# Kernel optimization log

Measured on AMD Instinct MI355X. Metric: run time of the kernel, lower is better.

The kernel has to match this reference:

```python
import jax, jax.numpy as jnp
import numpy as np
import math

B, C, D, NH, L, DFF = 128, 112, 512, 8, 13, 1920
DK = D // NH  # 64
_pos = np.arange(64)
_ranks, _files = _pos // 8, _pos % 8
RIDX = np.clip(_ranks[:, None] - _ranks[None, :], -7, 7) + 7  # [64,64] rel-rank bucket
FIDX = np.clip(_files[:, None] - _files[None, :], -7, 7) + 7  # [64,64] rel-file bucket
DIAG = _ranks + _files        # [64] in [0,14]
ADIAG = _ranks - _files + 7   # [64] in [0,14]


def _ln(x, g, b):
    m = jnp.mean(x, -1, keepdims=True)
    v = jnp.mean((x - m) ** 2, -1, keepdims=True)
    return (x - m) * jax.lax.rsqrt(v + 1e-5) * g + b


def setup_inputs() -> dict:
    key = jax.random.key(0)
    ks = iter(jax.random.split(key, 40))
    nrm = lambda *s: jax.random.normal(next(ks), s, jnp.float32) * 0.02
    return dict(
        x=jax.random.normal(next(ks), (B, C, 8, 8), jnp.float32),
        conv_w=nrm(C, D), conv_b=jnp.zeros(D),
        cls_token=nrm(1, 1, D),
        abs_pos=nrm(1, 64, D),
        file_emb=nrm(8, D), rank_emb=nrm(8, D),
        diag_emb=nrm(15, D), anti_diag_emb=nrm(15, D),
        ln1_g=jnp.ones((L, D)), ln1_b=jnp.zeros((L, D)),
        wq=nrm(L, D, D), bq=jnp.zeros((L, D)),
        wk=nrm(L, D, D), bk=jnp.zeros((L, D)),
        wv=nrm(L, D, D), bv=jnp.zeros((L, D)),
        wo=nrm(L, D, D), bo=jnp.zeros((L, D)),
        rel_bias=nrm(L, 15, 15, NH),
        ln2_g=jnp.ones((L, D)), ln2_b=jnp.zeros((L, D)),
        w_ff1=nrm(L, D, 2 * DFF), b_ff1=jnp.zeros((L, 2 * DFF)),
        w_ff2=nrm(L, DFF, D), b_ff2=jnp.zeros((L, D)),
        out_g=jnp.ones(D), out_b=jnp.zeros(D),
        vw1=nrm(D, D // 2), vb1=jnp.zeros(D // 2),
        vw2=nrm(D // 2, 128), vb2=jnp.zeros(128),
        vw3=nrm(128, 3), vb3=jnp.zeros(3),
        pw=nrm(D, 72), pb=jnp.zeros(72),
    )


def reference(x, conv_w, conv_b, cls_token, abs_pos, file_emb, rank_emb, diag_emb, anti_diag_emb,
              ln1_g, ln1_b, wq, bq, wk, bk, wv, bv, wo, bo, rel_bias, ln2_g, ln2_b,
              w_ff1, b_ff1, w_ff2, b_ff2, out_g, out_b,
              vw1, vb1, vw2, vb2, vw3, vb3, pw, pb):
    Bc = x.shape[0]
    # 1x1 conv == channel-wise linear; flatten spatial (row-major: s = rank*8 + file)
    tok = jnp.einsum('bcs,cd->bsd', x.reshape(Bc, C, 64), conv_w) + conv_b  # [B,64,D]
    pos = abs_pos + file_emb[_files] + rank_emb[_ranks] + diag_emb[DIAG] + anti_diag_emb[ADIAG]
    tok = tok + pos
    h = jnp.concatenate([jnp.broadcast_to(cls_token, (Bc, 1, D)), tok], axis=1)  # [B,65,D]
    scale = 1.0 / math.sqrt(DK)

    def block(hx, p):
        g1, b1, Wq, Bq, Wk, Bk, Wv, Bv, Wo, Bo, rb, g2, b2, W1, B1, W2, B2 = p
        n = _ln(hx, g1, b1)
        q = (n @ Wq + Bq).reshape(Bc, 65, NH, DK).transpose(0, 2, 1, 3)
        k = (n @ Wk + Bk).reshape(Bc, 65, NH, DK).transpose(0, 2, 1, 3)
        v = (n @ Wv + Bv).reshape(Bc, 65, NH, DK).transpose(0, 2, 1, 3)
        # gather relative-position bias [64,64,H] -> [H,65,65] with zero row/col for CLS
        bias = jnp.pad(jnp.transpose(rb[RIDX, FIDX], (2, 0, 1)), ((0, 0), (1, 0), (1, 0)))
        scores = jnp.einsum('bhqd,bhkd->bhqk', q, k) * scale + bias[None]
        a = jax.nn.softmax(scores, axis=-1)
        ctx = jnp.einsum('bhqk,bhkd->bhqd', a, v).transpose(0, 2, 1, 3).reshape(Bc, 65, D)
        hx = hx + ctx @ Wo + Bo
        n2 = _ln(hx, g2, b2)
        u = n2 @ W1 + B1
        u1, u2 = jnp.split(u, 2, axis=-1)
        hx = hx + (jax.nn.gelu(u1, approximate=False) * u2) @ W2 + B2
        return hx, None

    params = (ln1_g, ln1_b, wq, bq, wk, bk, wv, bv, wo, bo, rel_bias,
              ln2_g, ln2_b, w_ff1, b_ff1, w_ff2, b_ff2)
    h, _ = jax.lax.scan(block, h, params)
    h = _ln(h, out_g, out_b)
    cls = h[:, 0]
    v1 = jax.nn.gelu(cls @ vw1 + vb1, approximate=False)
    v2 = jax.nn.gelu(v1 @ vw2 + vb2, approximate=False)
    value = v2 @ vw3 + vb3                 # WDL logits [B,3]
    policy = (h[:, 1:] @ pw + pb).reshape(Bc, -1)  # [B, 64*72]
    return policy, value
```

## Files before the change

### kernel.cpp

```cpp
#include <hip/hip_runtime.h>
#include <stdint.h>

#define NLAYER 13
#define DMODEL 512
#define SEQ    65
#define BATCH  128
#define MROWS  (BATCH*SEQ)
#define NHEAD  8
#define DFFH   1920

typedef __bf16 bf16x8 __attribute__((ext_vector_type(8)));
typedef float  f32x4  __attribute__((ext_vector_type(4)));

__device__ __forceinline__ float bf2f(unsigned short u) {
    union { unsigned int i; float f; } c; c.i = ((unsigned int)u) << 16; return c.f;
}
__device__ __forceinline__ unsigned short f2bf(float f) {
    union { float f; unsigned int i; } c; c.f = f;
    unsigned int u = c.i;
    u += 0x7fffu + ((u >> 16) & 1u);
    return (unsigned short)(u >> 16);
}
__device__ __forceinline__ float gelu_exact(float x) {
    return 0.5f * x * (1.0f + erff(x * 0.70710678118654752f));
}

#define GLOAD16(gp, lp) __builtin_amdgcn_global_load_lds( \
    (const __attribute__((address_space(1))) unsigned int*)(gp), \
    (__attribute__((address_space(3))) unsigned int*)(lp), 16, 0, 0)

__global__ __launch_bounds__(256) void transpose_f32_bf16(
    const float* __restrict__ src, unsigned short* __restrict__ dst,
    int R, int C, int Cpad, long srcLS, long dstLS, int rowOff)
{
    __shared__ float tile[32][33];
    int l  = blockIdx.z;
    int c0 = blockIdx.x * 32, r0 = blockIdx.y * 32;
    const float* s = src + (long)l * srcLS;
    unsigned short* d = dst + (long)l * dstLS;
    int tx = threadIdx.x, ty = threadIdx.y;
#pragma unroll
    for (int k = 0; k < 4; k++) {
        int r = r0 + ty + 8*k, c = c0 + tx;
        float v = (r < R && c < C) ? s[(long)r * C + c] : 0.0f;
        tile[ty + 8*k][tx] = v;
    }
    __syncthreads();
#pragma unroll
    for (int k = 0; k < 4; k++) {
        int c = c0 + ty + 8*k, r = r0 + tx;
        if (c < Cpad && r < R)
            d[(long)(rowOff + c) * R + r] = f2bf(tile[tx][ty + 8*k]);
    }
}

__global__ __launch_bounds__(256) void stack_bias_kernel(
    const float* __restrict__ bq, const float* __restrict__ bk,
    const float* __restrict__ bv, float* __restrict__ bqkv)
{
    int idx = blockIdx.x * 256 + threadIdx.x;
    if (idx >= NLAYER * 1536) return;
    int l = idx / 1536, r = idx - l * 1536;
    float v;
    if (r < 512)       v = bq[l*512 + r];
    else if (r < 1024) v = bk[l*512 + r - 512];
    else               v = bv[l*512 + r - 1024];
    bqkv[idx] = v;
}

__global__ __launch_bounds__(256) void embed_kernel(
    const float* __restrict__ x, const float* __restrict__ conv_w,
    const float* __restrict__ conv_b, const float* __restrict__ cls_tok,
    const float* __restrict__ abs_pos, const float* __restrict__ file_emb,
    const float* __restrict__ rank_emb, const float* __restrict__ diag_emb,
    const float* __restrict__ adiag_emb, float* __restrict__ h)
{
    int b = blockIdx.y, sg = blockIdx.x, t = threadIdx.x;
    if (sg == 8) {
        for (int d = t; d < 512; d += 256)
            h[(long)b * SEQ * 512 + d] = cls_tok[d];
        return;
    }
    __shared__ float xs[112][8];
    for (int idx = t; idx < 112*8; idx += 256) {
        int c = idx >> 3, j = idx & 7;
        xs[c][j] = x[((long)b*112 + c)*64 + sg*8 + j];
    }
    __syncthreads();
    int d0 = t, d1 = t + 256;
    float acc0[8] = {}, acc1[8] = {};
    for (int c = 0; c < 112; c++) {
        float w0 = conv_w[c*512 + d0], w1 = conv_w[c*512 + d1];
#pragma unroll
        for (int j = 0; j < 8; j++) { acc0[j] += xs[c][j]*w0; acc1[j] += xs[c][j]*w1; }
    }
#pragma unroll
    for (int j = 0; j < 8; j++) {
        int sq = sg*8 + j, r = sq >> 3, f = sq & 7;
        long row = ((long)b * SEQ + 1 + sq) * 512;
        h[row + d0] = acc0[j] + conv_b[d0] + abs_pos[sq*512+d0] + file_emb[f*512+d0]
                    + rank_emb[r*512+d0] + diag_emb[(r+f)*512+d0] + adiag_emb[(r-f+7)*512+d0];
        h[row + d1] = acc1[j] + conv_b[d1] + abs_pos[sq*512+d1] + file_emb[f*512+d1]
                    + rank_emb[r*512+d1] + diag_emb[(r+f)*512+d1] + adiag_emb[(r-f+7)*512+d1];
    }
}

__global__ __launch_bounds__(256) void ln_kernel(
    const float* __restrict__ hx, const float* __restrict__ g,
    const float* __restrict__ bb, unsigned short* __restrict__ o)
{
    int row  = blockIdx.x * 4 + (threadIdx.x >> 6);
    int lane = threadIdx.x & 63;
    const float4* xr = (const float4*)(hx + (long)row * 512);
    float4 v0 = xr[lane], v1 = xr[lane + 64];
    float s  = v0.x+v0.y+v0.z+v0.w + v1.x+v1.y+v1.z+v1.w;
    float s2 = v0.x*v0.x+v0.y*v0.y+v0.z*v0.z+v0.w*v0.w
             + v1.x*v1.x+v1.y*v1.y+v1.z*v1.z+v1.w*v1.w;
    for (int off = 32; off; off >>= 1) { s += __shfl_xor(s, off); s2 += __shfl_xor(s2, off); }
    float mean = s * (1.0f/512.0f);
    float var  = s2 * (1.0f/512.0f) - mean*mean;
    float rs   = rsqrtf(var + 1e-5f);
    const float4* gr = (const float4*)g; const float4* br = (const float4*)bb;
    float4 g0 = gr[lane], g1 = gr[lane+64], b0 = br[lane], b1 = br[lane+64];
    ushort4 o0, o1;
    o0.x = f2bf((v0.x-mean)*rs*g0.x + b0.x);
    o0.y = f2bf((v0.y-mean)*rs*g0.y + b0.y);
    o0.z = f2bf((v0.z-mean)*rs*g0.z + b0.z);
    o0.w = f2bf((v0.w-mean)*rs*g0.w + b0.w);
    o1.x = f2bf((v1.x-mean)*rs*g1.x + b1.x);
    o1.y = f2bf((v1.y-mean)*rs*g1.y + b1.y);
    o1.z = f2bf((v1.z-mean)*rs*g1.z + b1.z);
    o1.w = f2bf((v1.w-mean)*rs*g1.w + b1.w);
    ushort4* orow = (ushort4*)(o + (long)row * 512);
    orow[lane] = o0; orow[lane + 64] = o1;
}

template<int MODE>
__global__ __launch_bounds__(256) void gemm128(
    const unsigned short* __restrict__ A, const unsigned short* __restrict__ Bt,
    const float* __restrict__ bias, const float* __restrict__ res,
    void* __restrict__ out, int K, int ldo)
{
    __shared__ __attribute__((aligned(16))) unsigned short As[128*32];
    __shared__ __attribute__((aligned(16))) unsigned short Bs[128*32];
    int m0 = blockIdx.y * 128;
    int bn = blockIdx.x;
    int tid = threadIdx.x;
    int lane = tid & 63, w = tid >> 6;
    int quad = lane >> 4, col = lane & 15;

    int srow = tid >> 2;
    int sc8  = (tid & 3) * 8;

    int br0, br1;
    if (MODE == 2) {
        br0 = bn*64 + srow;
        br1 = 1920 + bn*64 + srow;
    } else {
        br0 = bn*128 + srow;
        br1 = bn*128 + srow + 64;
    }
    const unsigned short* Arow0 = A + (long)(m0 + srow) * K + sc8;
    const unsigned short* Arow1 = A + (long)(m0 + srow + 64) * K + sc8;
    const unsigned short* Brow0 = Bt + (long)br0 * K + sc8;
    const unsigned short* Brow1 = Bt + (long)br1 * K + sc8;
    unsigned short* lAs0 = &As[srow*32 + sc8];
    unsigned short* lAs1 = &As[(srow+64)*32 + sc8];
    unsigned short* lBs0 = &Bs[srow*32 + sc8];
    unsigned short* lBs1 = &Bs[(srow+64)*32 + sc8];

    f32x4 acc[2][8] = {};

    for (int k0 = 0; k0 < K; k0 += 32) {
        GLOAD16(Arow0 + k0, lAs0);
        GLOAD16(Arow1 + k0, lAs1);
        GLOAD16(Brow0 + k0, lBs0);
        GLOAD16(Brow1 + k0, lBs1);
        __syncthreads();
        bf16x8 af[2], bfr[8];
#pragma unroll
        for (int i = 0; i < 2; i++)
            af[i] = *(const bf16x8*)(&As[(w*32 + i*16 + col)*32 + quad*8]);
#pragma unroll
        for (int t = 0; t < 8; t++)
            bfr[t] = *(const bf16x8*)(&Bs[(t*16 + col)*32 + quad*8]);
#pragma unroll
        for (int i = 0; i < 2; i++)
#pragma unroll
            for (int t = 0; t < 8; t++)
                acc[i][t] = __builtin_amdgcn_mfma_f32_16x16x32_bf16(af[i], bfr[t], acc[i][t], 0, 0, 0);
        __syncthreads();
    }

    if (MODE == 2) {
        unsigned short* O = (unsigned short*)out;
        int gn0 = bn * 64;
#pragma unroll
        for (int i = 0; i < 2; i++)
#pragma unroll
        for (int t = 0; t < 4; t++) {
            int c = t*16 + col;
            float b1v = bias[gn0 + c];
            float b2v = bias[1920 + gn0 + c];
#pragma unroll
            for (int r = 0; r < 4; r++) {
                int m = m0 + w*32 + i*16 + quad*4 + r;
                float u1 = acc[i][t][r]   + b1v;
                float u2 = acc[i][t+4][r] + b2v;
                O[(long)m * DFFH + gn0 + c] = f2bf(gelu_exact(u1) * u2);
            }
        }
        return;
    }
    int n0 = bn * 128;
#pragma unroll
    for (int i = 0; i < 2; i++)
#pragma unroll
    for (int t = 0; t < 8; t++) {
        int cg = n0 + t*16 + col;
        float bv = (MODE == 3) ? (cg < 72 ? bias[cg] : 0.0f) : bias[cg];
#pragma unroll
        for (int r = 0; r < 4; r++) {
            int m = m0 + w*32 + i*16 + quad*4 + r;
            float v = acc[i][t][r] + bv;
            if (MODE == 0) {
                ((unsigned short*)out)[(long)m * ldo + cg] = f2bf(v);
            } else if (MODE == 1) {
                ((float*)out)[(long)m * ldo + cg] = res[(long)m * ldo + cg] + v;
            } else {
                if (cg < 72) {
                    int b2 = m / 65, s = m - b2 * 65;
                    if (s > 0)
                        ((float*)out)[(long)b2 * 4608 + (s - 1) * 72 + cg] = v;
                }
            }
        }
    }
}

__global__ __launch_bounds__(256) void attn_mfma_kernel(
    const unsigned short* __restrict__ qkv,
    const float* __restrict__ rel_bias,
    unsigned short* __restrict__ ctx,
    int layer)
{
    constexpr int QS = 72;
    constexpr int VS = 104;
    constexpr int SS = 68;
    constexpr int PS = 104;
    __shared__ __attribute__((aligned(16))) unsigned short Qs[80*QS];
    __shared__ __attribute__((aligned(16))) unsigned short Ks[80*QS];
    __shared__ __attribute__((aligned(16))) unsigned short Vt[64*VS];
    __shared__ __attribute__((aligned(16))) float Sf[65*SS];
    __shared__ __attribute__((aligned(16))) unsigned short Pb[80*PS];
    __shared__ float bias_s[225];

    int h = blockIdx.x, b = blockIdx.y, t = threadIdx.x;
    int lane = t & 63, w = t >> 6;
    int quad = lane >> 4, col = lane & 15;

    for (int i = t; i < 225; i += 256)
        bias_s[i] = rel_bias[((long)layer*225 + i)*8 + h];

    for (int i = t; i < 65*8; i += 256) {
        int s = i >> 3, c8 = (i & 7) * 8;
        const unsigned short* row = qkv + ((long)(b*65+s))*1536 + h*64 + c8;
        int4 qv = *(const int4*)(row);
        int4 kv = *(const int4*)(row + 512);
        int4 vv = *(const int4*)(row + 1024);
        unsigned short qsc[8];
        const unsigned short* qp = (const unsigned short*)&qv;
#pragma unroll
        for (int j = 0; j < 8; j++) qsc[j] = f2bf(bf2f(qp[j]) * 0.125f);
        *(int4*)&Qs[s*QS + c8] = *(const int4*)qsc;
        *(int4*)&Ks[s*QS + c8] = kv;
        const unsigned short* vp = (const unsigned short*)&vv;
#pragma unroll
        for (int j = 0; j < 8; j++) Vt[(c8+j)*VS + s] = vp[j];
    }
    for (int i = t; i < 64*31; i += 256) {
        int d = i / 31, s = 65 + i % 31;
        Vt[d*VS + s] = 0;
    }
    __syncthreads();

    for (int tt = w; tt < 25; tt += 4) {
        int mi = tt / 5, nj = tt % 5;
        f32x4 acc = {};
        bf16x8 a0 = *(const bf16x8*)&Qs[(mi*16+col)*QS + quad*8];
        bf16x8 b0 = *(const bf16x8*)&Ks[(nj*16+col)*QS + quad*8];
        acc = __builtin_amdgcn_mfma_f32_16x16x32_bf16(a0, b0, acc, 0, 0, 0);
        bf16x8 a1 = *(const bf16x8*)&Qs[(mi*16+col)*QS + 32 + quad*8];
        bf16x8 b1 = *(const bf16x8*)&Ks[(nj*16+col)*QS + 32 + quad*8];
        acc = __builtin_amdgcn_mfma_f32_16x16x32_bf16(a1, b1, acc, 0, 0, 0);
#pragma unroll
        for (int r = 0; r < 4; r++) {
            int qi = mi*16 + quad*4 + r, kj = nj*16 + col;
            if (qi < 65 && kj < 65) {
                float v = acc[r];
                if (qi >= 1 && kj >= 1) {
                    int i2 = qi - 1, j2 = kj - 1;
                    int dr = (i2 >> 3) - (j2 >> 3) + 7;
                    int df = (i2 & 7) - (j2 & 7) + 7;
                    v += bias_s[dr*15 + df];
                }
                Sf[qi*SS + kj] = v;
            }
        }
    }
    __syncthreads();

    for (int r = w; r < 65; r += 4) {
        float x0 = Sf[r*SS + lane];
        float x1 = (lane == 0) ? Sf[r*SS + 64] : -1e30f;
        float mx = fmaxf(x0, x1);
        for (int off = 32; off; off >>= 1) mx = fmaxf(mx, __shfl_xor(mx, off));
        float e0 = __expf(x0 - mx);
        float e1 = (lane == 0) ? __expf(x1 - mx) : 0.0f;
        float sm = e0 + e1;
        for (int off = 32; off; off >>= 1) sm += __shfl_xor(sm, off);
        float inv = 1.0f / sm;
        Pb[r*PS + lane] = f2bf(e0 * inv);
        if (lane == 0)  Pb[r*PS + 64] = f2bf(e1 * inv);
        if (lane >= 1 && lane <= 31) Pb[r*PS + 64 + lane] = 0;
    }
    __syncthreads();

    for (int tt = w; tt < 20; tt += 4) {
        int mi = tt >> 2, dj = tt & 3;
        f32x4 acc = {};
#pragma unroll
        for (int ks = 0; ks < 3; ks++) {
            bf16x8 a  = *(const bf16x8*)&Pb[(mi*16+col)*PS + ks*32 + quad*8];
            bf16x8 bb = *(const bf16x8*)&Vt[(dj*16+col)*VS + ks*32 + quad*8];
            acc = __builtin_amdgcn_mfma_f32_16x16x32_bf16(a, bb, acc, 0, 0, 0);
        }
#pragma unroll
        for (int r = 0; r < 4; r++) {
            int qi = mi*16 + quad*4 + r;
            if (qi < 65)
                ctx[((long)(b*65+qi))*512 + h*64 + dj*16 + col] = f2bf(acc[r]);
        }
    }
}

__global__ __launch_bounds__(256) void value_head_kernel(
    const unsigned short* __restrict__ hn,
    const float* __restrict__ vw1, const float* __restrict__ vb1,
    const float* __restrict__ vw2, const float* __restrict__ vb2,
    const float* __restrict__ vw3, const float* __restrict__ vb3,
    float* __restrict__ outv)
{
    int b = blockIdx.x, t = threadIdx.x;
    __shared__ float cls[512], v1[256], v2[128];
    for (int d = t; d < 512; d += 256) cls[d] = bf2f(hn[(long)b * SEQ * 512 + d]);
    __syncthreads();
    {
        float a = vb1[t];
        for (int c = 0; c < 512; c++) a += cls[c] * vw1[c*256 + t];
        v1[t] = gelu_exact(a);
    }
    __syncthreads();
    if (t < 128) {
        float a = vb2[t];
        for (int c = 0; c < 256; c++) a += v1[c] * vw2[c*128 + t];
        v2[t] = gelu_exact(a);
    }
    __syncthreads();
    if (t < 3) {
        float a = vb3[t];
        for (int c = 0; c < 128; c++) a += v2[c] * vw3[c*3 + t];
        outv[b*3 + t] = a;
    }
}

extern "C" void kernel_launch(void* const* d_in, const int* in_sizes, int n_in,
                              void* d_out, int out_size, void* d_ws, size_t ws_size,
                              hipStream_t stream)
{
    (void)in_sizes; (void)n_in; (void)out_size; (void)ws_size;
    const float* x        = (const float*)d_in[0];
    const float* conv_w   = (const float*)d_in[1];
    const float* conv_b   = (const float*)d_in[2];
    const float* cls_tok  = (const float*)d_in[3];
    const float* abs_pos  = (const float*)d_in[4];
    const float* file_emb = (const float*)d_in[5];
    const float* rank_emb = (const float*)d_in[6];
    const float* diag_emb = (const float*)d_in[7];
    const float* adiag    = (const float*)d_in[8];
    const float* ln1_g    = (const float*)d_in[9];
    const float* ln1_b    = (const float*)d_in[10];
    const float* wq       = (const float*)d_in[11];
    const float* bq       = (const float*)d_in[12];
    const float* wk       = (const float*)d_in[13];
    const float* bk       = (const float*)d_in[14];
    const float* wv       = (const float*)d_in[15];
    const float* bv       = (const float*)d_in[16];
    const float* wo       = (const float*)d_in[17];
    const float* bo       = (const float*)d_in[18];
    const float* rel_bias = (const float*)d_in[19];
    const float* ln2_g    = (const float*)d_in[20];
    const float* ln2_b    = (const float*)d_in[21];
    const float* w_ff1    = (const float*)d_in[22];
    const float* b_ff1    = (const float*)d_in[23];
    const float* w_ff2    = (const float*)d_in[24];
    const float* b_ff2    = (const float*)d_in[25];
    const float* out_g    = (const float*)d_in[26];
    const float* out_b    = (const float*)d_in[27];
    const float* vw1      = (const float*)d_in[28];
    const float* vb1      = (const float*)d_in[29];
    const float* vw2      = (const float*)d_in[30];
    const float* vb2      = (const float*)d_in[31];
    const float* vw3      = (const float*)d_in[32];
    const float* vb3      = (const float*)d_in[33];
    const float* pw       = (const float*)d_in[34];
    const float* pb       = (const float*)d_in[35];

    char* p = (char*)d_ws;
    auto alloc = [&](size_t bytes) { void* r = (void*)p; p += (bytes + 255) & ~(size_t)255; return r; };
    unsigned short* qkvT = (unsigned short*)alloc((size_t)NLAYER*1536*512*2);
    unsigned short* woT  = (unsigned short*)alloc((size_t)NLAYER*512*512*2);
    unsigned short* w1T  = (unsigned short*)alloc((size_t)NLAYER*3840*512*2);
    unsigned short* w2T  = (unsigned short*)alloc((size_t)NLAYER*512*1920*2);
    unsigned short* pwT  = (unsigned short*)alloc((size_t)128*512*2);
    float*          bqkv = (float*)alloc((size_t)NLAYER*1536*4);
    float*          h    = (float*)alloc((size_t)MROWS*512*4);
    unsigned short* nbf  = (unsigned short*)alloc((size_t)MROWS*512*2);
    unsigned short* qkvb = (unsigned short*)alloc((size_t)MROWS*1536*2);
    unsigned short* ctxb = (unsigned short*)alloc((size_t)MROWS*512*2);
    unsigned short* gbuf = (unsigned short*)alloc((size_t)MROWS*1920*2);

    dim3 tb(32, 8);
    transpose_f32_bf16<<<dim3(16,16,NLAYER), tb, 0, stream>>>(wq, qkvT, 512, 512, 512, 512L*512, 1536L*512, 0);
    transpose_f32_bf16<<<dim3(16,16,NLAYER), tb, 0, stream>>>(wk, qkvT, 512, 512, 512, 512L*512, 1536L*512, 512);
    transpose_f32_bf16<<<dim3(16,16,NLAYER), tb, 0, stream>>>(wv, qkvT, 512, 512, 512, 512L*512, 1536L*512, 1024);
    transpose_f32_bf16<<<dim3(16,16,NLAYER), tb, 0, stream>>>(wo, woT, 512, 512, 512, 512L*512, 512L*512, 0);
    transpose_f32_bf16<<<dim3(120,16,NLAYER), tb, 0, stream>>>(w_ff1, w1T, 512, 3840, 3840, 512L*3840, 3840L*512, 0);
    transpose_f32_bf16<<<dim3(16,60,NLAYER), tb, 0, stream>>>(w_ff2, w2T, 1920, 512, 512, 1920L*512, 512L*1920, 0);
    transpose_f32_bf16<<<dim3(4,16,1), tb, 0, stream>>>(pw, pwT, 512, 72, 128, 0, 0, 0);
    stack_bias_kernel<<<(NLAYER*1536 + 255)/256, 256, 0, stream>>>(bq, bk, bv, bqkv);

    embed_kernel<<<dim3(9, BATCH), 256, 0, stream>>>(x, conv_w, conv_b, cls_tok, abs_pos,
                                                     file_emb, rank_emb, diag_emb, adiag, h);

    for (int l = 0; l < NLAYER; l++) {
        ln_kernel<<<MROWS/4, 256, 0, stream>>>(h, ln1_g + l*512, ln1_b + l*512, nbf);
        gemm128<0><<<dim3(12,65), 256, 0, stream>>>(nbf, qkvT + (size_t)l*1536*512,
                                                    bqkv + l*1536, nullptr, qkvb, 512, 1536);
        attn_mfma_kernel<<<dim3(NHEAD, BATCH), 256, 0, stream>>>(qkvb, rel_bias, ctxb, l);
        gemm128<1><<<dim3(4,65), 256, 0, stream>>>(ctxb, woT + (size_t)l*512*512,
                                                   bo + l*512, h, h, 512, 512);
        ln_kernel<<<MROWS/4, 256, 0, stream>>>(h, ln2_g + l*512, ln2_b + l*512, nbf);
        gemm128<2><<<dim3(30,65), 256, 0, stream>>>(nbf, w1T + (size_t)l*3840*512,
                                                    b_ff1 + l*3840, nullptr, gbuf, 512, 0);
        gemm128<1><<<dim3(4,65), 256, 0, stream>>>(gbuf, w2T + (size_t)l*512*1920,
                                                   b_ff2 + l*512, h, h, 1920, 512);
    }

    ln_kernel<<<MROWS/4, 256, 0, stream>>>(h, out_g, out_b, nbf);
    gemm128<3><<<dim3(1,65), 256, 0, stream>>>(nbf, pwT, pb, nullptr, (float*)d_out, 512, 0);
    value_head_kernel<<<BATCH, 256, 0, stream>>>(nbf, vw1, vb1, vw2, vb2, vw3, vb3,
                                                 (float*)d_out + (size_t)BATCH*4608);
}
```

Baseline: 3.161 ms.

## Register-prefetch GEMM tiles and remap blocks into per-XCD M bands

Replaces the direct global-to-LDS loads with register staging: the next K-slice is loaded into registers while MFMAs run on the current LDS tile, so global latency overlaps with compute. It also flattens the grid and maps block IDs so that each of the 8 XCDs owns a contiguous band of M tiles, aiming for better L2 reuse of A rows within an XCD. The costs are extra VGPRs, an extra LDS store per K-step, and 7 idle padding blocks per N column.

```diff
diff --git a/kernel.cpp b/kernel.cpp
--- a/kernel.cpp
+++ b/kernel.cpp
@@ -8,6 +8,8 @@
 #define MROWS  (BATCH*SEQ)
 #define NHEAD  8
 #define DFFH   1920
+#define MTILES 65
+#define MBAND  9
 
 typedef __bf16 bf16x8 __attribute__((ext_vector_type(8)));
 typedef float  f32x4  __attribute__((ext_vector_type(4)));
@@ -24,10 +26,6 @@
 __device__ __forceinline__ float gelu_exact(float x) {
     return 0.5f * x * (1.0f + erff(x * 0.70710678118654752f));
 }
-
-#define GLOAD16(gp, lp) __builtin_amdgcn_global_load_lds( \
-    (const __attribute__((address_space(1))) unsigned int*)(gp), \
-    (__attribute__((address_space(3))) unsigned int*)(lp), 16, 0, 0)
 
 __global__ __launch_bounds__(256) void transpose_f32_bf16(
     const float* __restrict__ src, unsigned short* __restrict__ dst,
@@ -139,12 +137,16 @@
 __global__ __launch_bounds__(256) void gemm128(
     const unsigned short* __restrict__ A, const unsigned short* __restrict__ Bt,
     const float* __restrict__ bias, const float* __restrict__ res,
-    void* __restrict__ out, int K, int ldo)
+    void* __restrict__ out, int K, int ldo, int nT)
 {
     __shared__ __attribute__((aligned(16))) unsigned short As[128*32];
     __shared__ __attribute__((aligned(16))) unsigned short Bs[128*32];
-    int m0 = blockIdx.y * 128;
-    int bn = blockIdx.x;
+    int id = blockIdx.x;
+    int xcd = id & 7, jj = id >> 3;
+    int bn  = jj % nT;
+    int mt  = xcd * MBAND + jj / nT;
+    if (mt >= MTILES) return;
+    int m0 = mt * 128;
     int tid = threadIdx.x;
     int lane = tid & 63, w = tid >> 6;
     int quad = lane >> 4, col = lane & 15;
@@ -164,19 +166,28 @@
     const unsigned short* Arow1 = A + (long)(m0 + srow + 64) * K + sc8;
     const unsigned short* Brow0 = Bt + (long)br0 * K + sc8;
     const unsigned short* Brow1 = Bt + (long)br1 * K + sc8;
-    unsigned short* lAs0 = &As[srow*32 + sc8];
-    unsigned short* lAs1 = &As[(srow+64)*32 + sc8];
-    unsigned short* lBs0 = &Bs[srow*32 + sc8];
-    unsigned short* lBs1 = &Bs[(srow+64)*32 + sc8];
 
     f32x4 acc[2][8] = {};
 
+    int4 ca0 = *(const int4*)(Arow0);
+    int4 ca1 = *(const int4*)(Arow1);
+    int4 cb0 = *(const int4*)(Brow0);
+    int4 cb1 = *(const int4*)(Brow1);
+
     for (int k0 = 0; k0 < K; k0 += 32) {
-        GLOAD16(Arow0 + k0, lAs0);
-        GLOAD16(Arow1 + k0, lAs1);
-        GLOAD16(Brow0 + k0, lBs0);
-        GLOAD16(Brow1 + k0, lBs1);
         __syncthreads();
+        *(int4*)(&As[srow*32 + sc8])        = ca0;
+        *(int4*)(&As[(srow+64)*32 + sc8])   = ca1;
+        *(int4*)(&Bs[srow*32 + sc8])        = cb0;
+        *(int4*)(&Bs[(srow+64)*32 + sc8])   = cb1;
+        __syncthreads();
+        int kn = k0 + 32;
+        if (kn < K) {
+            ca0 = *(const int4*)(Arow0 + kn);
+            ca1 = *(const int4*)(Arow1 + kn);
+            cb0 = *(const int4*)(Brow0 + kn);
+            cb1 = *(const int4*)(Brow1 + kn);
+        }
         bf16x8 af[2], bfr[8];
 #pragma unroll
         for (int i = 0; i < 2; i++)
@@ -189,7 +200,6 @@
 #pragma unroll
             for (int t = 0; t < 8; t++)
                 acc[i][t] = __builtin_amdgcn_mfma_f32_16x16x32_bf16(af[i], bfr[t], acc[i][t], 0, 0, 0);
-        __syncthreads();
     }
 
     if (MODE == 2) {
@@ -445,20 +455,20 @@
 
     for (int l = 0; l < NLAYER; l++) {
         ln_kernel<<<MROWS/4, 256, 0, stream>>>(h, ln1_g + l*512, ln1_b + l*512, nbf);
-        gemm128<0><<<dim3(12,65), 256, 0, stream>>>(nbf, qkvT + (size_t)l*1536*512,
-                                                    bqkv + l*1536, nullptr, qkvb, 512, 1536);
+        gemm128<0><<<72*12, 256, 0, stream>>>(nbf, qkvT + (size_t)l*1536*512,
+                                              bqkv + l*1536, nullptr, qkvb, 512, 1536, 12);
         attn_mfma_kernel<<<dim3(NHEAD, BATCH), 256, 0, stream>>>(qkvb, rel_bias, ctxb, l);
-        gemm128<1><<<dim3(4,65), 256, 0, stream>>>(ctxb, woT + (size_t)l*512*512,
-                                                   bo + l*512, h, h, 512, 512);
+        gemm128<1><<<72*4, 256, 0, stream>>>(ctxb, woT + (size_t)l*512*512,
+                                             bo + l*512, h, h, 512, 512, 4);
         ln_kernel<<<MROWS/4, 256, 0, stream>>>(h, ln2_g + l*512, ln2_b + l*512, nbf);
-        gemm128<2><<<dim3(30,65), 256, 0, stream>>>(nbf, w1T + (size_t)l*3840*512,
-                                                    b_ff1 + l*3840, nullptr, gbuf, 512, 0);
-        gemm128<1><<<dim3(4,65), 256, 0, stream>>>(gbuf, w2T + (size_t)l*512*1920,
-                                                   b_ff2 + l*512, h, h, 1920, 512);
+        gemm128<2><<<72*30, 256, 0, stream>>>(nbf, w1T + (size_t)l*3840*512,
+                                              b_ff1 + l*3840, nullptr, gbuf, 512, 0, 30);
+        gemm128<1><<<72*4, 256, 0, stream>>>(gbuf, w2T + (size_t)l*512*1920,
+                                             b_ff2 + l*512, h, h, 1920, 512, 4);
     }
 
     ln_kernel<<<MROWS/4, 256, 0, stream>>>(h, out_g, out_b, nbf);
-    gemm128<3><<<dim3(1,65), 256, 0, stream>>>(nbf, pwT, pb, nullptr, (float*)d_out, 512, 0);
+    gemm128<3><<<72*1, 256, 0, stream>>>(nbf, pwT, pb, nullptr, (float*)d_out, 512, 0, 1);
     value_head_kernel<<<BATCH, 256, 0, stream>>>(nbf, vw1, vb1, vw2, vb2, vw3, vb3,
                                                  (float*)d_out + (size_t)BATCH*4608);
 }
```

Result: faster. 2.874 ms (-9.1%).
